# Optimization experiments

Measured on AMD Instinct MI355X. Metric: run time of the kernel, lower is better.

## Reference

```python
import jax, jax.numpy as jnp
import numpy as np

W_SCALE = 0.05  # keep gates out of hard saturation


def _lstm_dir(x_tbd, Wih, Whh, b, reverse):
    """One direction of one LSTM layer. x_tbd: [T,B,Din]. Returns hs [T,B,H]."""
    H = Whh.shape[1]
    B = x_tbd.shape[1]
    # precompute input projections for all timesteps: [T,B,4H]
    xp = jnp.einsum('tbd,gd->tbg', x_tbd, Wih) + b
    if reverse:
        xp = xp[::-1]

    def step(carry, xg):
        h, c = carry
        gates = xg + h @ Whh.T  # [B,4H], PyTorch gate order i,f,g,o
        i, f, g, o = jnp.split(gates, 4, axis=-1)
        i = jax.nn.sigmoid(i)
        f = jax.nn.sigmoid(f)
        g = jnp.tanh(g)
        o = jax.nn.sigmoid(o)
        c = f * c + i * g
        h = o * jnp.tanh(c)
        return (h, c), h

    h0 = jnp.zeros((B, H), dtype=x_tbd.dtype)
    c0 = jnp.zeros((B, H), dtype=x_tbd.dtype)
    _, hs = jax.lax.scan(step, (h0, c0), xp)
    if reverse:
        hs = hs[::-1]
    return hs


def setup_inputs() -> dict:
    key = jax.random.key(0)
    ks = jax.random.split(key, 8)
    B, T, V, E, H, L = 32, 512, 32000, 1024, 512, 2
    inp = jax.random.randint(ks[0], (B, T), 0, V)
    emb = jax.random.normal(ks[1], (V, E), dtype=jnp.float32) * W_SCALE
    Wih = jax.random.normal(ks[2], (L, 2, 4 * H, E), dtype=jnp.float32) * W_SCALE
    Whh = jax.random.normal(ks[3], (L, 2, 4 * H, H), dtype=jnp.float32) * W_SCALE
    bih = jax.random.normal(ks[4], (L, 2, 4 * H), dtype=jnp.float32) * W_SCALE
    bhh = jax.random.normal(ks[5], (L, 2, 4 * H), dtype=jnp.float32) * W_SCALE
    Wout = jax.random.normal(ks[6], (1, 2 * H), dtype=jnp.float32) * W_SCALE
    bout = jax.random.normal(ks[7], (1,), dtype=jnp.float32) * W_SCALE
    return {"inp": inp, "emb": emb, "Wih": Wih, "Whh": Whh,
            "bih": bih, "bhh": bhh, "Wout": Wout, "bout": bout}


def reference(inp, emb, Wih, Whh, bih, bhh, Wout, bout):
    H = Whh.shape[-1]
    L = Wih.shape[0]
    x = emb[inp]                      # [B,T,E] embedding lookup
    x = jnp.transpose(x, (1, 0, 2))   # [T,B,E] time-major for scan
    for l in range(L):
        b_f = bih[l, 0] + bhh[l, 0]
        b_r = bih[l, 1] + bhh[l, 1]
        h_f = _lstm_dir(x, Wih[l, 0], Whh[l, 0], b_f, reverse=False)
        h_r = _lstm_dir(x, Wih[l, 1], Whh[l, 1], b_r, reverse=True)
        x = jnp.concatenate([h_f, h_r], axis=-1)  # [T,B,2H]
        # dropout between layers is identity in eval mode
    vec = jnp.transpose(x, (1, 0, 2))  # [B,T,2H]
    nor_out = vec[:, -1, :H]           # last step of forward direction
    rev_out = vec[:, 0, H:]            # first step of reverse direction
    pooled = jnp.concatenate([nor_out, rev_out], axis=1)  # [B,2H]
    out = pooled @ Wout.T + bout       # [B,1]
    return jnp.squeeze(out, axis=-1)   # [B]
```

## Files before the change

kernel.cpp:

```cpp
#include <hip/hip_runtime.h>
#include <stdint.h>

typedef unsigned short u16;
typedef unsigned int u32;
typedef __attribute__((ext_vector_type(8))) short short8;
typedef __attribute__((ext_vector_type(4))) float f32x4;

#define T_SEQ 512
#define NB 32
#define EMBD 1024
#define HID 512
#define G4 2048
#define NROWS (T_SEQ * NB)
#define XPW 4096
#define WPD 32
#define SENTW 0xFFFFFFFFu

static __device__ __forceinline__ u16 f2bf(float x) {
  unsigned u = __float_as_uint(x);
  u += 0x7fffu + ((u >> 16) & 1u);
  return (u16)(u >> 16);
}
static __device__ __forceinline__ float bf2f(u16 b) {
  return __uint_as_float(((unsigned)b) << 16);
}
static __device__ __forceinline__ f32x4 mfma16(short8 a, short8 b, f32x4 c) {
  return __builtin_amdgcn_mfma_f32_16x16x32_bf16(a, b, c, 0, 0, 0);
}
static __device__ __forceinline__ float fast_tanh(float x) {
  float e = __expf(2.f * x);
  return 1.f - 2.f / (e + 1.f);
}
static __device__ __forceinline__ float sigm(float x) {
  return 1.f / (1.f + __expf(-x));
}
static __device__ __forceinline__ void barrier_lds() {
  asm volatile("s_waitcnt lgkmcnt(0)" ::: "memory");
  __builtin_amdgcn_s_barrier();
  asm volatile("" ::: "memory");
}

__global__ void k_prep(const float* __restrict__ Wih, const float* __restrict__ Whh,
                       const float* __restrict__ bih, const float* __restrict__ bhh,
                       u16* __restrict__ wih_b, u16* __restrict__ whh_hi,
                       u16* __restrict__ whh_lo, float* __restrict__ bcat) {
  size_t stride = (size_t)gridDim.x * blockDim.x;
  size_t i0 = (size_t)blockIdx.x * blockDim.x + threadIdx.x;
  const size_t n_ih = (size_t)2 * 2 * G4 * EMBD;
  for (size_t i = i0; i < n_ih; i += stride) wih_b[i] = f2bf(Wih[i]);
  const size_t n_hh = (size_t)2 * 2 * G4 * HID;
  for (size_t i = i0; i < n_hh; i += stride) {
    float w = Whh[i];
    u16 hi = f2bf(w);
    whh_hi[i] = hi;
    whh_lo[i] = f2bf(w - bf2f(hi));
  }
  for (size_t i = i0; i < 2 * 4096; i += stride) {
    size_t l = i >> 12, col = i & 4095;
    bcat[i] = bih[l * 4096 + col] + bhh[l * 4096 + col];
  }
}

__global__ void k_gather(const int* __restrict__ inp, const float* __restrict__ emb,
                         u16* __restrict__ X) {
  int row = blockIdx.x;
  int t = row >> 5, b = row & 31;
  int tok = inp[b * T_SEQ + t];
  const float* src = emb + (size_t)tok * EMBD + threadIdx.x * 4;
  float4 v = *reinterpret_cast<const float4*>(src);
  ushort4 o;
  o.x = f2bf(v.x); o.y = f2bf(v.y); o.z = f2bf(v.z); o.w = f2bf(v.w);
  *reinterpret_cast<ushort4*>(X + (size_t)row * EMBD + threadIdx.x * 4) = o;
}

#define GBM 128
#define GBN 128
#define GBK 64
__global__ __launch_bounds__(256) void k_gemm(const u16* __restrict__ A,
                                              const u16* __restrict__ B,
                                              const float* __restrict__ bias,
                                              u16* __restrict__ C) {
  __shared__ u16 As[GBM][GBK];
  __shared__ u16 Bs[GBN][GBK];
  const int Kdim = 1024, Ndim = 4096;
  int bm = blockIdx.x, bn = blockIdx.y;
  int tid = threadIdx.x;
  int lane = tid & 63, wave = tid >> 6;
  int wm = wave >> 1, wn = wave & 1;
  int l15 = lane & 15, klo = (lane >> 4) * 8;
  f32x4 acc[4][4] = {};
  for (int k0 = 0; k0 < Kdim; k0 += GBK) {
#pragma unroll
    for (int s = 0; s < 4; s++) {
      int seg = tid + s * 256;
      int r = seg >> 3, cs = (seg & 7) * 8;
      *reinterpret_cast<short8*>(&As[r][cs]) =
          *reinterpret_cast<const short8*>(A + (size_t)(bm * GBM + r) * Kdim + k0 + cs);
      *reinterpret_cast<short8*>(&Bs[r][cs]) =
          *reinterpret_cast<const short8*>(B + (size_t)(bn * GBN + r) * Kdim + k0 + cs);
    }
    __syncthreads();
#pragma unroll
    for (int kk = 0; kk < GBK; kk += 32) {
      short8 af[4], bfb[4];
#pragma unroll
      for (int i = 0; i < 4; i++)
        af[i] = *reinterpret_cast<const short8*>(&As[wm * 64 + i * 16 + l15][kk + klo]);
#pragma unroll
      for (int j = 0; j < 4; j++)
        bfb[j] = *reinterpret_cast<const short8*>(&Bs[wn * 64 + j * 16 + l15][kk + klo]);
#pragma unroll
      for (int i = 0; i < 4; i++)
#pragma unroll
        for (int j = 0; j < 4; j++)
          acc[i][j] = mfma16(af[i], bfb[j], acc[i][j]);
    }
    __syncthreads();
  }
  int lg4 = (lane >> 4) * 4;
#pragma unroll
  for (int i = 0; i < 4; i++) {
#pragma unroll
    for (int j = 0; j < 4; j++) {
      int n = bn * GBN + wn * 64 + j * 16 + l15;
      float bv = bias[n];
#pragma unroll
      for (int r = 0; r < 4; r++) {
        int m = bm * GBM + wm * 64 + i * 16 + lg4 + r;
        C[(size_t)m * Ndim + n] = f2bf(acc[i][j][r] + bv);
      }
    }
  }
}

__global__ __launch_bounds__(256, 1) void k_lstm8(const u16* __restrict__ xp,
                                                  const u16* __restrict__ whh_hi,
                                                  const u16* __restrict__ whh_lo,
                                                  u32* __restrict__ ypk,
                                                  u16* __restrict__ yh,
                                                  int write_yh) {
  int blk = blockIdx.x;
  int dir = blk >> 5, slice = blk & 31;
  int tid = threadIdx.x, wave = tid >> 6, lane = tid & 63;
  int u0 = slice * 16;
  int l15 = lane & 15, lg = lane >> 4;
  int klo = lg * 8;

  f32x4 whf[4][4], wlf[4][4];
#pragma unroll
  for (int ct = 0; ct < 4; ct++) {
    size_t wr = ((size_t)dir * G4 + ct * HID + u0 + l15) * HID + wave * 128 + klo;
#pragma unroll
    for (int kt = 0; kt < 4; kt++) {
      whf[ct][kt] = *reinterpret_cast<const f32x4*>(whh_hi + wr + kt * 32);
      wlf[ct][kt] = *reinterpret_cast<const f32x4*>(whh_lo + wr + kt * 32);
    }
  }
#pragma unroll
  for (int ct = 0; ct < 4; ct++)
#pragma unroll
    for (int kt = 0; kt < 4; kt++) {
      asm volatile("" : "+v"(whf[ct][kt]));
      asm volatile("" : "+v"(wlf[ct][kt]));
    }

  __shared__ float pgx[4][NB][16][5];
  float cst[2] = {0.f, 0.f};
  int bj[2], uj[2];
#pragma unroll
  for (int j = 0; j < 2; j++) {
    int p = tid + 256 * j;
    uj[j] = p & 15;
    bj[j] = p >> 4;
  }

  for (int s = 0; s < T_SEQ; s++) {
    int trow = dir ? (T_SEQ - 1 - s) : s;
    short8 ah[2][4], al[2][4];
    if (s > 0) {
      int prow = dir ? (T_SEQ - s) : (s - 1);
      const u32* yb = ypk + ((size_t)prow * NB + l15) * 1024 + dir * HID + wave * 128 + klo;
      uint4 hb[2][4][2];
      while (true) {
#pragma unroll
        for (int mt = 0; mt < 2; mt++) {
          const u32* pb = yb + (size_t)mt * 16 * 1024;
#pragma unroll
          for (int kt = 0; kt < 4; kt++) {
            asm volatile("global_load_dwordx4 %0, %1, off offset:%2 sc0 sc1"
                         : "=&v"(hb[mt][kt][0]) : "v"(pb), "i"(kt * 128));
            asm volatile("global_load_dwordx4 %0, %1, off offset:%2 sc0 sc1"
                         : "=&v"(hb[mt][kt][1]) : "v"(pb), "i"(kt * 128 + 16));
          }
        }
        asm volatile("s_waitcnt vmcnt(0)" ::: "memory");
        __builtin_amdgcn_sched_barrier(0);
        u32 mx = 0;
#pragma unroll
        for (int mt = 0; mt < 2; mt++)
#pragma unroll
          for (int kt = 0; kt < 4; kt++)
#pragma unroll
            for (int h2 = 0; h2 < 2; h2++) {
              uint4 v = hb[mt][kt][h2];
              mx = max(mx, max(max(v.x, v.y), max(v.z, v.w)));
            }
        if (__all(mx != SENTW)) break;
      }
#pragma unroll
      for (int mt = 0; mt < 2; mt++)
#pragma unroll
        for (int kt = 0; kt < 4; kt++) {
          uint4 a = hb[mt][kt][0], b = hb[mt][kt][1];
          u32 v8[8] = {a.x, a.y, a.z, a.w, b.x, b.y, b.z, b.w};
          union { short8 s8; u32 u[4]; } uh, ul;
#pragma unroll
          for (int i = 0; i < 4; i++) {
            uh.u[i] = __builtin_amdgcn_perm(v8[2 * i + 1], v8[2 * i], 0x07060302u);
            ul.u[i] = __builtin_amdgcn_perm(v8[2 * i + 1], v8[2 * i], 0x05040100u);
          }
          ah[mt][kt] = uh.s8;
          al[mt][kt] = ul.s8;
        }
    }
    u32 xqr[2][4];
#pragma unroll
    for (int j = 0; j < 2; j++) {
      const u16* xb = xp + (size_t)(trow * NB + bj[j]) * XPW + dir * 2048 + u0 + uj[j];
#pragma unroll
      for (int g = 0; g < 4; g++)
        asm volatile("global_load_ushort %0, %1, off offset:%2"
                     : "=&v"(xqr[j][g]) : "v"(xb), "i"(g * HID * 2));
    }
    if (s > 0) {
      f32x4 accM[2][4], accC[2][4];
#pragma unroll
      for (int mt = 0; mt < 2; mt++)
#pragma unroll
        for (int ct = 0; ct < 4; ct++) {
          accM[mt][ct] = (f32x4){0.f, 0.f, 0.f, 0.f};
          accC[mt][ct] = (f32x4){0.f, 0.f, 0.f, 0.f};
        }
#pragma unroll
      for (int kt = 0; kt < 4; kt++)
#pragma unroll
        for (int mt = 0; mt < 2; mt++)
#pragma unroll
          for (int ct = 0; ct < 4; ct++) {
            short8 wh = __builtin_bit_cast(short8, whf[ct][kt]);
            short8 wl = __builtin_bit_cast(short8, wlf[ct][kt]);
            accM[mt][ct] = mfma16(ah[mt][kt], wh, accM[mt][ct]);
            accC[mt][ct] = mfma16(al[mt][kt], wh, accC[mt][ct]);
            accC[mt][ct] = mfma16(ah[mt][kt], wl, accC[mt][ct]);
          }
#pragma unroll
      for (int mt = 0; mt < 2; mt++)
#pragma unroll
        for (int ct = 0; ct < 4; ct++) {
          f32x4 v4 = accM[mt][ct] + accC[mt][ct];
#pragma unroll
          for (int r = 0; r < 4; r++)
            pgx[ct][mt * 16 + lg * 4 + r][l15][wave] = v4[r];
        }
    }
    barrier_lds();
    asm volatile("s_waitcnt vmcnt(0)" ::: "memory");
    __builtin_amdgcn_sched_barrier(0);
#pragma unroll
    for (int j = 0; j < 2; j++) {
      int b = bj[j], uu = uj[j];
      float gs[4];
#pragma unroll
      for (int g = 0; g < 4; g++) {
        float v = bf2f((u16)xqr[j][g]);
        if (s > 0)
          v += (pgx[g][b][uu][0] + pgx[g][b][uu][1]) +
               (pgx[g][b][uu][2] + pgx[g][b][uu][3]);
        gs[g] = v;
      }
      float iv = sigm(gs[0]);
      float fv = sigm(gs[1]);
      float gv = fast_tanh(gs[2]);
      float ov = sigm(gs[3]);
      float c = fv * cst[j] + iv * gv;
      cst[j] = c;
      float h = ov * fast_tanh(c);
      u16 hh = f2bf(h);
      u16 hl = f2bf(h - bf2f(hh));
      size_t yo = ((size_t)trow * NB + b) * 1024 + dir * HID + u0 + uu;
      __hip_atomic_store(ypk + yo, ((u32)hh << 16) | hl, __ATOMIC_RELAXED,
                         __HIP_MEMORY_SCOPE_AGENT);
      if (write_yh) yh[yo] = hh;
    }
    barrier_lds();
  }
}

__global__ void k_out(const u32* __restrict__ ypk, const float* __restrict__ wout,
                      const float* __restrict__ bout, float* __restrict__ out) {
  int b = blockIdx.x;
  __shared__ float red[256];
  float s = 0.f;
  for (int c = threadIdx.x; c < 1024; c += 256) {
    size_t row = (c < 512) ? ((size_t)(T_SEQ - 1) * NB + b) : (size_t)b;
    u32 pk = ypk[row * 1024 + c];
    float h = bf2f((u16)(pk >> 16)) + bf2f((u16)(pk & 0xFFFFu));
    s += h * wout[c];
  }
  red[threadIdx.x] = s;
  __syncthreads();
  for (int st = 128; st > 0; st >>= 1) {
    if (threadIdx.x < st) red[threadIdx.x] += red[threadIdx.x + st];
    __syncthreads();
  }
  if (threadIdx.x == 0) out[b] = red[0] + bout[0];
}

extern "C" void kernel_launch(void* const* d_in, const int* in_sizes, int n_in,
                              void* d_out, int out_size, void* d_ws, size_t ws_size,
                              hipStream_t stream) {
  const int*   inp  = (const int*)d_in[0];
  const float* emb  = (const float*)d_in[1];
  const float* Wih  = (const float*)d_in[2];
  const float* Whh  = (const float*)d_in[3];
  const float* bih  = (const float*)d_in[4];
  const float* bhh  = (const float*)d_in[5];
  const float* Wout = (const float*)d_in[6];
  const float* bout = (const float*)d_in[7];
  float* out = (float*)d_out;
  char* ws = (char*)d_ws;

  const size_t SZ_XP  = (size_t)NROWS * XPW * 2;
  const size_t SZ_YPK = (size_t)NROWS * 1024 * 4;
  const size_t SZ_YH  = (size_t)NROWS * 1024 * 2;
  const size_t SZ_WIH = (size_t)2 * 4096 * 1024 * 2;
  const size_t SZ_WHH = (size_t)2 * 2 * G4 * HID * 2;
  size_t off = 0;
  auto alloc = [&](size_t n) { size_t o = off; off += (n + 255) & ~(size_t)255; return o; };
  size_t o_xp   = alloc(SZ_XP);
  size_t o_ypkA = alloc(SZ_YPK);
  size_t o_y1h  = alloc(SZ_YH);
  size_t o_x1   = alloc(SZ_YH);
  size_t o_wih  = alloc(SZ_WIH);
  size_t o_whhh = alloc(SZ_WHH);
  size_t o_whhl = alloc(SZ_WHH);
  size_t o_bc   = alloc(2 * 4096 * sizeof(float));
  if (ws_size < off) return;

  u16* xp   = (u16*)(ws + o_xp);
  u32* ypkA = (u32*)(ws + o_ypkA);
  u16* y1h  = (u16*)(ws + o_y1h);
  u16* x1   = (u16*)(ws + o_x1);
  u32* ypkB = (u32*)(ws + o_y1h);
  u16* wihb = (u16*)(ws + o_wih);
  u16* whhh = (u16*)(ws + o_whhh);
  u16* whhl = (u16*)(ws + o_whhl);
  float* bc = (float*)(ws + o_bc);

  hipMemsetAsync(ypkA, 0xFF, SZ_YPK, stream);
  k_prep<<<4096, 256, 0, stream>>>(Wih, Whh, bih, bhh, wihb, whhh, whhl, bc);
  k_gather<<<NROWS, 256, 0, stream>>>(inp, emb, x1);
  k_gemm<<<dim3(NROWS / GBM, XPW / GBN), 256, 0, stream>>>(x1, wihb, bc, xp);
  k_lstm8<<<2 * WPD, 256, 0, stream>>>(xp, whhh, whhl, ypkA, y1h, 1);
  k_gemm<<<dim3(NROWS / GBM, XPW / GBN), 256, 0, stream>>>(
      y1h, wihb + (size_t)4096 * 1024, bc + 4096, xp);
  hipMemsetAsync(ypkB, 0xFF, SZ_YPK, stream);
  k_lstm8<<<2 * WPD, 256, 0, stream>>>(xp, whhh + (size_t)2 * G4 * HID,
                                       whhl + (size_t)2 * G4 * HID, ypkB, y1h, 0);
  k_out<<<NB, 256, 0, stream>>>(ypkB, Wout, bout, out);
}
```

Measured before the change: 5.380 ms.

## Co-locate LSTM blocks per XCD and poll h via XCD-local L2

Launches 256 blocks and keeps only those with blockIdx%8 in {0,1}, so that under round-robin XCD dispatch all forward-direction blocks share one XCD and all reverse-direction blocks share another. The cross-block spin-wait on the recurrent state then reads with sc0 only (L2-coherent within the XCD) rather than sc0 sc1 (system level), and each h value is stored twice: a plain store that fills the local L2 and an sc0 sc1 store for coherence. After 256 failed polls it falls back to the LLC-coherent loads. The goal is lower per-step synchronization latency, but correctness relies on the undocumented block-to-XCD mapping, the double stores add write traffic, and 192 empty blocks are launched.

```diff
diff --git a/kernel.cpp b/kernel.cpp
--- a/kernel.cpp
+++ b/kernel.cpp
@@ -133,14 +133,16 @@
   }
 }
 
-__global__ __launch_bounds__(256, 1) void k_lstm8(const u16* __restrict__ xp,
+__global__ __launch_bounds__(256, 1) void k_lstm9(const u16* __restrict__ xp,
                                                   const u16* __restrict__ whh_hi,
                                                   const u16* __restrict__ whh_lo,
                                                   u32* __restrict__ ypk,
                                                   u16* __restrict__ yh,
                                                   int write_yh) {
   int blk = blockIdx.x;
-  int dir = blk >> 5, slice = blk & 31;
+  int role = blk & 7;
+  if (role > 1) return;
+  int dir = role, slice = blk >> 3;
   int tid = threadIdx.x, wave = tid >> 6, lane = tid & 63;
   int u0 = slice * 16;
   int l15 = lane & 15, lg = lane >> 4;
@@ -173,6 +175,7 @@
     uj[j] = p & 15;
     bj[j] = p >> 4;
   }
+  int use_llc = 0;
 
   for (int s = 0; s < T_SEQ; s++) {
     int trow = dir ? (T_SEQ - 1 - s) : s;
@@ -181,16 +184,31 @@
       int prow = dir ? (T_SEQ - s) : (s - 1);
       const u32* yb = ypk + ((size_t)prow * NB + l15) * 1024 + dir * HID + wave * 128 + klo;
       uint4 hb[2][4][2];
+      int tries = 0;
       while (true) {
-#pragma unroll
-        for (int mt = 0; mt < 2; mt++) {
-          const u32* pb = yb + (size_t)mt * 16 * 1024;
-#pragma unroll
-          for (int kt = 0; kt < 4; kt++) {
-            asm volatile("global_load_dwordx4 %0, %1, off offset:%2 sc0 sc1"
-                         : "=&v"(hb[mt][kt][0]) : "v"(pb), "i"(kt * 128));
-            asm volatile("global_load_dwordx4 %0, %1, off offset:%2 sc0 sc1"
-                         : "=&v"(hb[mt][kt][1]) : "v"(pb), "i"(kt * 128 + 16));
+        if (!use_llc) {
+#pragma unroll
+          for (int mt = 0; mt < 2; mt++) {
+            const u32* pb = yb + (size_t)mt * 16 * 1024;
+#pragma unroll
+            for (int kt = 0; kt < 4; kt++) {
+              asm volatile("global_load_dwordx4 %0, %1, off offset:%2 sc0"
+                           : "=&v"(hb[mt][kt][0]) : "v"(pb), "i"(kt * 128));
+              asm volatile("global_load_dwordx4 %0, %1, off offset:%2 sc0"
+                           : "=&v"(hb[mt][kt][1]) : "v"(pb), "i"(kt * 128 + 16));
+            }
+          }
+        } else {
+#pragma unroll
+          for (int mt = 0; mt < 2; mt++) {
+            const u32* pb = yb + (size_t)mt * 16 * 1024;
+#pragma unroll
+            for (int kt = 0; kt < 4; kt++) {
+              asm volatile("global_load_dwordx4 %0, %1, off offset:%2 sc0 sc1"
+                           : "=&v"(hb[mt][kt][0]) : "v"(pb), "i"(kt * 128));
+              asm volatile("global_load_dwordx4 %0, %1, off offset:%2 sc0 sc1"
+                           : "=&v"(hb[mt][kt][1]) : "v"(pb), "i"(kt * 128 + 16));
+            }
           }
         }
         asm volatile("s_waitcnt vmcnt(0)" ::: "memory");
@@ -206,6 +224,7 @@
               mx = max(mx, max(max(v.x, v.y), max(v.z, v.w)));
             }
         if (__all(mx != SENTW)) break;
+        if (++tries == 256) use_llc = 1;
       }
 #pragma unroll
       for (int mt = 0; mt < 2; mt++)
@@ -288,8 +307,10 @@
       u16 hh = f2bf(h);
       u16 hl = f2bf(h - bf2f(hh));
       size_t yo = ((size_t)trow * NB + b) * 1024 + dir * HID + u0 + uu;
-      __hip_atomic_store(ypk + yo, ((u32)hh << 16) | hl, __ATOMIC_RELAXED,
-                         __HIP_MEMORY_SCOPE_AGENT);
+      u32 pkv = ((u32)hh << 16) | hl;
+      u32* addr = ypk + yo;
+      asm volatile("global_store_dword %0, %1, off" :: "v"(addr), "v"(pkv) : "memory");
+      asm volatile("global_store_dword %0, %1, off sc0 sc1" :: "v"(addr), "v"(pkv) : "memory");
       if (write_yh) yh[yo] = hh;
     }
     barrier_lds();
@@ -361,11 +382,11 @@
   k_prep<<<4096, 256, 0, stream>>>(Wih, Whh, bih, bhh, wihb, whhh, whhl, bc);
   k_gather<<<NROWS, 256, 0, stream>>>(inp, emb, x1);
   k_gemm<<<dim3(NROWS / GBM, XPW / GBN), 256, 0, stream>>>(x1, wihb, bc, xp);
-  k_lstm8<<<2 * WPD, 256, 0, stream>>>(xp, whhh, whhl, ypkA, y1h, 1);
+  k_lstm9<<<256, 256, 0, stream>>>(xp, whhh, whhl, ypkA, y1h, 1);
   k_gemm<<<dim3(NROWS / GBM, XPW / GBN), 256, 0, stream>>>(
       y1h, wihb + (size_t)4096 * 1024, bc + 4096, xp);
   hipMemsetAsync(ypkB, 0xFF, SZ_YPK, stream);
-  k_lstm8<<<2 * WPD, 256, 0, stream>>>(xp, whhh + (size_t)2 * G4 * HID,
-                                       whhl + (size_t)2 * G4 * HID, ypkB, y1h, 0);
+  k_lstm9<<<256, 256, 0, stream>>>(xp, whhh + (size_t)2 * G4 * HID,
+                                   whhl + (size_t)2 * G4 * HID, ypkB, y1h, 0);
   k_out<<<NB, 256, 0, stream>>>(ypkB, Wout, bout, out);
 }
```

Measured after the change: 8.772 ms. 63.0% more time.

## Process both LSTM directions in one block per slice and read packed hidden states in GEMM

Applied to the files above, without the earlier changes.

The recurrent kernel now launches 32 blocks instead of 64, and each block holds the Whh slices for both directions in registers, interleaving forward and reverse steps inside one loop. The layer-2 input GEMM reads the packed hi/lo ypk buffer directly and extracts the high bf16 half, so the separate yh write is gone. The two MFMA accumulators are merged into one. This halves the block count but doubles the serial per-block work and the register pressure. Each step still has its own sentinel spin wait, so latency is likely to grow unless the two directions overlap well.

```diff
diff --git a/kernel.cpp b/kernel.cpp
--- a/kernel.cpp
+++ b/kernel.cpp
@@ -13,7 +13,7 @@
 #define G4 2048
 #define NROWS (T_SEQ * NB)
 #define XPW 4096
-#define WPD 32
+#define NSLICE 32
 #define SENTW 0xFFFFFFFFu
 
 static __device__ __forceinline__ u16 f2bf(float x) {
@@ -76,7 +76,8 @@
 #define GBM 128
 #define GBN 128
 #define GBK 64
-__global__ __launch_bounds__(256) void k_gemm(const u16* __restrict__ A,
+template <int PACKED>
+__global__ __launch_bounds__(256) void k_gemm(const void* __restrict__ Av,
                                               const u16* __restrict__ B,
                                               const float* __restrict__ bias,
                                               u16* __restrict__ C) {
@@ -94,8 +95,20 @@
     for (int s = 0; s < 4; s++) {
       int seg = tid + s * 256;
       int r = seg >> 3, cs = (seg & 7) * 8;
-      *reinterpret_cast<short8*>(&As[r][cs]) =
-          *reinterpret_cast<const short8*>(A + (size_t)(bm * GBM + r) * Kdim + k0 + cs);
+      if (PACKED) {
+        const u32* srcp = (const u32*)Av + (size_t)(bm * GBM + r) * Kdim + k0 + cs;
+        uint4 a = *reinterpret_cast<const uint4*>(srcp);
+        uint4 b = *reinterpret_cast<const uint4*>(srcp + 4);
+        uint4 o;
+        o.x = __builtin_amdgcn_perm(a.y, a.x, 0x07060302u);
+        o.y = __builtin_amdgcn_perm(a.w, a.z, 0x07060302u);
+        o.z = __builtin_amdgcn_perm(b.y, b.x, 0x07060302u);
+        o.w = __builtin_amdgcn_perm(b.w, b.z, 0x07060302u);
+        *reinterpret_cast<uint4*>(&As[r][cs]) = o;
+      } else {
+        *reinterpret_cast<short8*>(&As[r][cs]) = *reinterpret_cast<const short8*>(
+            (const u16*)Av + (size_t)(bm * GBM + r) * Kdim + k0 + cs);
+      }
       *reinterpret_cast<short8*>(&Bs[r][cs]) =
           *reinterpret_cast<const short8*>(B + (size_t)(bn * GBN + r) * Kdim + k0 + cs);
     }
@@ -133,39 +146,40 @@
   }
 }
 
-__global__ __launch_bounds__(256, 1) void k_lstm8(const u16* __restrict__ xp,
-                                                  const u16* __restrict__ whh_hi,
-                                                  const u16* __restrict__ whh_lo,
-                                                  u32* __restrict__ ypk,
-                                                  u16* __restrict__ yh,
-                                                  int write_yh) {
-  int blk = blockIdx.x;
-  int dir = blk >> 5, slice = blk & 31;
+__global__ __launch_bounds__(256, 1) void k_lstm14(const u16* __restrict__ xp,
+                                                   const u16* __restrict__ whh_hi,
+                                                   const u16* __restrict__ whh_lo,
+                                                   u32* __restrict__ ypk) {
+  int slice = blockIdx.x;
   int tid = threadIdx.x, wave = tid >> 6, lane = tid & 63;
   int u0 = slice * 16;
   int l15 = lane & 15, lg = lane >> 4;
   int klo = lg * 8;
 
-  f32x4 whf[4][4], wlf[4][4];
-#pragma unroll
-  for (int ct = 0; ct < 4; ct++) {
-    size_t wr = ((size_t)dir * G4 + ct * HID + u0 + l15) * HID + wave * 128 + klo;
-#pragma unroll
-    for (int kt = 0; kt < 4; kt++) {
-      whf[ct][kt] = *reinterpret_cast<const f32x4*>(whh_hi + wr + kt * 32);
-      wlf[ct][kt] = *reinterpret_cast<const f32x4*>(whh_lo + wr + kt * 32);
-    }
-  }
-#pragma unroll
-  for (int ct = 0; ct < 4; ct++)
-#pragma unroll
-    for (int kt = 0; kt < 4; kt++) {
-      asm volatile("" : "+v"(whf[ct][kt]));
-      asm volatile("" : "+v"(wlf[ct][kt]));
-    }
+  f32x4 whf[2][4][4], wlf[2][4][4];
+#pragma unroll
+  for (int d = 0; d < 2; d++)
+#pragma unroll
+    for (int ct = 0; ct < 4; ct++) {
+      size_t wr = ((size_t)d * G4 + ct * HID + u0 + l15) * HID + wave * 128 + klo;
+#pragma unroll
+      for (int kt = 0; kt < 4; kt++) {
+        whf[d][ct][kt] = *reinterpret_cast<const f32x4*>(whh_hi + wr + kt * 32);
+        wlf[d][ct][kt] = *reinterpret_cast<const f32x4*>(whh_lo + wr + kt * 32);
+      }
+    }
+#pragma unroll
+  for (int d = 0; d < 2; d++)
+#pragma unroll
+    for (int ct = 0; ct < 4; ct++)
+#pragma unroll
+      for (int kt = 0; kt < 4; kt++) {
+        asm volatile("" : "+v"(whf[d][ct][kt]));
+        asm volatile("" : "+v"(wlf[d][ct][kt]));
+      }
 
   __shared__ float pgx[4][NB][16][5];
-  float cst[2] = {0.f, 0.f};
+  float cst[2][2] = {{0.f, 0.f}, {0.f, 0.f}};
   int bj[2], uj[2];
 #pragma unroll
   for (int j = 0; j < 2; j++) {
@@ -175,124 +189,121 @@
   }
 
   for (int s = 0; s < T_SEQ; s++) {
-    int trow = dir ? (T_SEQ - 1 - s) : s;
-    short8 ah[2][4], al[2][4];
-    if (s > 0) {
-      int prow = dir ? (T_SEQ - s) : (s - 1);
-      const u32* yb = ypk + ((size_t)prow * NB + l15) * 1024 + dir * HID + wave * 128 + klo;
-      uint4 hb[2][4][2];
-      while (true) {
-#pragma unroll
-        for (int mt = 0; mt < 2; mt++) {
-          const u32* pb = yb + (size_t)mt * 16 * 1024;
+#pragma unroll
+    for (int d = 0; d < 2; d++) {
+      int trow = d ? (T_SEQ - 1 - s) : s;
+      short8 ah[2][4], al[2][4];
+      if (s > 0) {
+        int prow = d ? (T_SEQ - s) : (s - 1);
+        const u32* yb = ypk + ((size_t)prow * NB + l15) * 1024 + d * HID + wave * 128 + klo;
+        uint4 hb[2][4][2];
+        while (true) {
+#pragma unroll
+          for (int mt = 0; mt < 2; mt++) {
+            const u32* pb = yb + (size_t)mt * 16 * 1024;
+#pragma unroll
+            for (int kt = 0; kt < 4; kt++) {
+              asm volatile("global_load_dwordx4 %0, %1, off offset:%2 sc0 sc1"
+                           : "=&v"(hb[mt][kt][0]) : "v"(pb), "i"(kt * 128));
+              asm volatile("global_load_dwordx4 %0, %1, off offset:%2 sc0 sc1"
+                           : "=&v"(hb[mt][kt][1]) : "v"(pb), "i"(kt * 128 + 16));
+            }
+          }
+          asm volatile("s_waitcnt vmcnt(0)" ::: "memory");
+          __builtin_amdgcn_sched_barrier(0);
+          u32 mx = 0;
+#pragma unroll
+          for (int mt = 0; mt < 2; mt++)
+#pragma unroll
+            for (int kt = 0; kt < 4; kt++)
+#pragma unroll
+              for (int h2 = 0; h2 < 2; h2++) {
+                uint4 v = hb[mt][kt][h2];
+                mx = max(mx, max(max(v.x, v.y), max(v.z, v.w)));
+              }
+          if (__all(mx != SENTW)) break;
+        }
+#pragma unroll
+        for (int mt = 0; mt < 2; mt++)
 #pragma unroll
           for (int kt = 0; kt < 4; kt++) {
-            asm volatile("global_load_dwordx4 %0, %1, off offset:%2 sc0 sc1"
-                         : "=&v"(hb[mt][kt][0]) : "v"(pb), "i"(kt * 128));
-            asm volatile("global_load_dwordx4 %0, %1, off offset:%2 sc0 sc1"
-                         : "=&v"(hb[mt][kt][1]) : "v"(pb), "i"(kt * 128 + 16));
+            uint4 a = hb[mt][kt][0], b = hb[mt][kt][1];
+            u32 v8[8] = {a.x, a.y, a.z, a.w, b.x, b.y, b.z, b.w};
+            union { short8 s8; u32 u[4]; } uh, ul;
+#pragma unroll
+            for (int i = 0; i < 4; i++) {
+              uh.u[i] = __builtin_amdgcn_perm(v8[2 * i + 1], v8[2 * i], 0x07060302u);
+              ul.u[i] = __builtin_amdgcn_perm(v8[2 * i + 1], v8[2 * i], 0x05040100u);
+            }
+            ah[mt][kt] = uh.s8;
+            al[mt][kt] = ul.s8;
           }
+      }
+      u32 xqr[2][4];
+#pragma unroll
+      for (int j = 0; j < 2; j++) {
+        const u16* xb = xp + (size_t)(trow * NB + bj[j]) * XPW + d * 2048 + u0 + uj[j];
+#pragma unroll
+        for (int g = 0; g < 4; g++)
+          asm volatile("global_load_ushort %0, %1, off offset:%2"
+                       : "=&v"(xqr[j][g]) : "v"(xb), "i"(g * HID * 2));
+      }
+      if (s > 0) {
+        f32x4 acc[2][4];
+#pragma unroll
+        for (int mt = 0; mt < 2; mt++)
+#pragma unroll
+          for (int ct = 0; ct < 4; ct++) acc[mt][ct] = (f32x4){0.f, 0.f, 0.f, 0.f};
+#pragma unroll
+        for (int kt = 0; kt < 4; kt++)
+#pragma unroll
+          for (int mt = 0; mt < 2; mt++)
+#pragma unroll
+            for (int ct = 0; ct < 4; ct++) {
+              short8 wh = __builtin_bit_cast(short8, whf[d][ct][kt]);
+              short8 wl = __builtin_bit_cast(short8, wlf[d][ct][kt]);
+              acc[mt][ct] = mfma16(ah[mt][kt], wh, acc[mt][ct]);
+              acc[mt][ct] = mfma16(al[mt][kt], wh, acc[mt][ct]);
+              acc[mt][ct] = mfma16(ah[mt][kt], wl, acc[mt][ct]);
+            }
+#pragma unroll
+        for (int mt = 0; mt < 2; mt++)
+#pragma unroll
+          for (int ct = 0; ct < 4; ct++)
+#pragma unroll
+            for (int r = 0; r < 4; r++)
+              pgx[ct][mt * 16 + lg * 4 + r][l15][wave] = acc[mt][ct][r];
+      }
+      barrier_lds();
+      asm volatile("s_waitcnt vmcnt(0)" ::: "memory");
+      __builtin_amdgcn_sched_barrier(0);
+#pragma unroll
+      for (int j = 0; j < 2; j++) {
+        int b = bj[j], uu = uj[j];
+        float gs[4];
+#pragma unroll
+        for (int g = 0; g < 4; g++) {
+          float v = bf2f((u16)xqr[j][g]);
+          if (s > 0)
+            v += (pgx[g][b][uu][0] + pgx[g][b][uu][1]) +
+                 (pgx[g][b][uu][2] + pgx[g][b][uu][3]);
+          gs[g] = v;
         }
-        asm volatile("s_waitcnt vmcnt(0)" ::: "memory");
-        __builtin_amdgcn_sched_barrier(0);
-        u32 mx = 0;
-#pragma unroll
-        for (int mt = 0; mt < 2; mt++)
-#pragma unroll
-          for (int kt = 0; kt < 4; kt++)
-#pragma unroll
-            for (int h2 = 0; h2 < 2; h2++) {
-              uint4 v = hb[mt][kt][h2];
-              mx = max(mx, max(max(v.x, v.y), max(v.z, v.w)));
-            }
-        if (__all(mx != SENTW)) break;
-      }
-#pragma unroll
-      for (int mt = 0; mt < 2; mt++)
-#pragma unroll
-        for (int kt = 0; kt < 4; kt++) {
-          uint4 a = hb[mt][kt][0], b = hb[mt][kt][1];
-          u32 v8[8] = {a.x, a.y, a.z, a.w, b.x, b.y, b.z, b.w};
-          union { short8 s8; u32 u[4]; } uh, ul;
-#pragma unroll
-          for (int i = 0; i < 4; i++) {
-            uh.u[i] = __builtin_amdgcn_perm(v8[2 * i + 1], v8[2 * i], 0x07060302u);
-            ul.u[i] = __builtin_amdgcn_perm(v8[2 * i + 1], v8[2 * i], 0x05040100u);
-          }
-          ah[mt][kt] = uh.s8;
-          al[mt][kt] = ul.s8;
-        }
-    }
-    u32 xqr[2][4];
-#pragma unroll
-    for (int j = 0; j < 2; j++) {
-      const u16* xb = xp + (size_t)(trow * NB + bj[j]) * XPW + dir * 2048 + u0 + uj[j];
-#pragma unroll
-      for (int g = 0; g < 4; g++)
-        asm volatile("global_load_ushort %0, %1, off offset:%2"
-                     : "=&v"(xqr[j][g]) : "v"(xb), "i"(g * HID * 2));
-    }
-    if (s > 0) {
-      f32x4 accM[2][4], accC[2][4];
-#pragma unroll
-      for (int mt = 0; mt < 2; mt++)
-#pragma unroll
-        for (int ct = 0; ct < 4; ct++) {
-          accM[mt][ct] = (f32x4){0.f, 0.f, 0.f, 0.f};
-          accC[mt][ct] = (f32x4){0.f, 0.f, 0.f, 0.f};
-        }
-#pragma unroll
-      for (int kt = 0; kt < 4; kt++)
-#pragma unroll
-        for (int mt = 0; mt < 2; mt++)
-#pragma unroll
-          for (int ct = 0; ct < 4; ct++) {
-            short8 wh = __builtin_bit_cast(short8, whf[ct][kt]);
-            short8 wl = __builtin_bit_cast(short8, wlf[ct][kt]);
-            accM[mt][ct] = mfma16(ah[mt][kt], wh, accM[mt][ct]);
-            accC[mt][ct] = mfma16(al[mt][kt], wh, accC[mt][ct]);
-            accC[mt][ct] = mfma16(ah[mt][kt], wl, accC[mt][ct]);
-          }
-#pragma unroll
-      for (int mt = 0; mt < 2; mt++)
-#pragma unroll
-        for (int ct = 0; ct < 4; ct++) {
-          f32x4 v4 = accM[mt][ct] + accC[mt][ct];
-#pragma unroll
-          for (int r = 0; r < 4; r++)
-            pgx[ct][mt * 16 + lg * 4 + r][l15][wave] = v4[r];
-        }
-    }
-    barrier_lds();
-    asm volatile("s_waitcnt vmcnt(0)" ::: "memory");
-    __builtin_amdgcn_sched_barrier(0);
-#pragma unroll
-    for (int j = 0; j < 2; j++) {
-      int b = bj[j], uu = uj[j];
-      float gs[4];
-#pragma unroll
-      for (int g = 0; g < 4; g++) {
-        float v = bf2f((u16)xqr[j][g]);
-        if (s > 0)
-          v += (pgx[g][b][uu][0] + pgx[g][b][uu][1]) +
-               (pgx[g][b][uu][2] + pgx[g][b][uu][3]);
-        gs[g] = v;
-      }
-      float iv = sigm(gs[0]);
-      float fv = sigm(gs[1]);
-      float gv = fast_tanh(gs[2]);
-      float ov = sigm(gs[3]);
-      float c = fv * cst[j] + iv * gv;
-      cst[j] = c;
-      float h = ov * fast_tanh(c);
-      u16 hh = f2bf(h);
-      u16 hl = f2bf(h - bf2f(hh));
-      size_t yo = ((size_t)trow * NB + b) * 1024 + dir * HID + u0 + uu;
-      __hip_atomic_store(ypk + yo, ((u32)hh << 16) | hl, __ATOMIC_RELAXED,
-                         __HIP_MEMORY_SCOPE_AGENT);
-      if (write_yh) yh[yo] = hh;
-    }
-    barrier_lds();
+        float iv = sigm(gs[0]);
+        float fv = sigm(gs[1]);
+        float gv = fast_tanh(gs[2]);
+        float ov = sigm(gs[3]);
+        float c = fv * cst[d][j] + iv * gv;
+        cst[d][j] = c;
+        float h = ov * fast_tanh(c);
+        u16 hh = f2bf(h);
+        u16 hl = f2bf(h - bf2f(hh));
+        size_t yo = ((size_t)trow * NB + b) * 1024 + d * HID + u0 + uu;
+        __hip_atomic_store(ypk + yo, ((u32)hh << 16) | hl, __ATOMIC_RELAXED,
+                           __HIP_MEMORY_SCOPE_AGENT);
+      }
+      barrier_lds();
+    }
   }
 }
 
@@ -332,15 +343,13 @@
 
   const size_t SZ_XP  = (size_t)NROWS * XPW * 2;
   const size_t SZ_YPK = (size_t)NROWS * 1024 * 4;
-  const size_t SZ_YH  = (size_t)NROWS * 1024 * 2;
   const size_t SZ_WIH = (size_t)2 * 4096 * 1024 * 2;
   const size_t SZ_WHH = (size_t)2 * 2 * G4 * HID * 2;
   size_t off = 0;
   auto alloc = [&](size_t n) { size_t o = off; off += (n + 255) & ~(size_t)255; return o; };
   size_t o_xp   = alloc(SZ_XP);
   size_t o_ypkA = alloc(SZ_YPK);
-  size_t o_y1h  = alloc(SZ_YH);
-  size_t o_x1   = alloc(SZ_YH);
+  size_t o_ypkB = alloc(SZ_YPK);
   size_t o_wih  = alloc(SZ_WIH);
   size_t o_whhh = alloc(SZ_WHH);
   size_t o_whhl = alloc(SZ_WHH);
@@ -349,23 +358,22 @@
 
   u16* xp   = (u16*)(ws + o_xp);
   u32* ypkA = (u32*)(ws + o_ypkA);
-  u16* y1h  = (u16*)(ws + o_y1h);
-  u16* x1   = (u16*)(ws + o_x1);
-  u32* ypkB = (u32*)(ws + o_y1h);
+  u32* ypkB = (u32*)(ws + o_ypkB);
+  u16* x1   = (u16*)(ws + o_ypkB);
   u16* wihb = (u16*)(ws + o_wih);
   u16* whhh = (u16*)(ws + o_whhh);
   u16* whhl = (u16*)(ws + o_whhl);
   float* bc = (float*)(ws + o_bc);
 
-  hipMemsetAsync(ypkA, 0xFF, SZ_YPK, stream);
+  (void)hipMemsetAsync(ypkA, 0xFF, SZ_YPK, stream);
   k_prep<<<4096, 256, 0, stream>>>(Wih, Whh, bih, bhh, wihb, whhh, whhl, bc);
   k_gather<<<NROWS, 256, 0, stream>>>(inp, emb, x1);
-  k_gemm<<<dim3(NROWS / GBM, XPW / GBN), 256, 0, stream>>>(x1, wihb, bc, xp);
-  k_lstm8<<<2 * WPD, 256, 0, stream>>>(xp, whhh, whhl, ypkA, y1h, 1);
-  k_gemm<<<dim3(NROWS / GBM, XPW / GBN), 256, 0, stream>>>(
-      y1h, wihb + (size_t)4096 * 1024, bc + 4096, xp);
-  hipMemsetAsync(ypkB, 0xFF, SZ_YPK, stream);
-  k_lstm8<<<2 * WPD, 256, 0, stream>>>(xp, whhh + (size_t)2 * G4 * HID,
-                                       whhl + (size_t)2 * G4 * HID, ypkB, y1h, 0);
+  k_gemm<0><<<dim3(NROWS / GBM, XPW / GBN), 256, 0, stream>>>(x1, wihb, bc, xp);
+  k_lstm14<<<NSLICE, 256, 0, stream>>>(xp, whhh, whhl, ypkA);
+  k_gemm<1><<<dim3(NROWS / GBM, XPW / GBN), 256, 0, stream>>>(
+      ypkA, wihb + (size_t)4096 * 1024, bc + 4096, xp);
+  (void)hipMemsetAsync(ypkB, 0xFF, SZ_YPK, stream);
+  k_lstm14<<<NSLICE, 256, 0, stream>>>(xp, whhh + (size_t)2 * G4 * HID,
+                                       whhl + (size_t)2 * G4 * HID, ypkB);
   k_out<<<NB, 256, 0, stream>>>(ypkB, Wout, bout, out);
 }
```

Result: slower. 8.734 ms (+62.3%).
